# Optimization experiments

Measured on AMD Instinct MI355X. Metric: run time of the kernel, lower is better.

Reference implementation:

```python
import jax, jax.numpy as jnp
import numpy as np

H = 128
N = 100_000
VOCAB = 15_128
LAYER_TIMESTEPS = [5, 2, 5, 2]
RESIDUALS = {1: [0], 3: [1]}


def gru_cell(x, h, Wih, Whh, bih, bhh):
    # torch.nn.GRUCell semantics
    gi = x @ Wih.T + bih
    gh = h @ Whh.T + bhh
    ir, iz, inn = jnp.split(gi, 3, axis=-1)
    hr, hz, hn = jnp.split(gh, 3, axis=-1)
    r = jax.nn.sigmoid(ir + hr)
    z = jax.nn.sigmoid(iz + hz)
    n = jnp.tanh(inn + r * hn)
    return (1.0 - z) * n + z * h


def setup_inputs() -> dict:
    key = jax.random.key(0)
    ks = jax.random.split(key, 12)
    E_AST, E_MASTER, V, P = 100_000, 20_000, 30_000, 8_000
    s = 1.0 / np.sqrt(H)
    inp = {
        "node_type_ids": jax.random.randint(ks[0], (N,), 0, VOCAB),
        "edges_ast": jax.random.randint(ks[1], (E_AST, 2), 0, N),
        "edges_master": jax.random.randint(ks[2], (E_MASTER, 2), 0, N),
        "var_node_pos": jax.random.randint(ks[3], (V,), 0, N),
        "pred_node_ids": jax.random.randint(ks[4], (P,), 0, N),
        # learned params
        "embedding": jax.random.normal(ks[5], (VOCAB, H), jnp.float32) * 0.02,
        "msg_W": jax.random.normal(ks[6], (4, 4, H, H), jnp.float32) * s,  # [layer, edge_type, H, H]
        "msg_b": jnp.zeros((4, 4, H), jnp.float32),
        "Wih_a": jax.random.normal(ks[7], (2, 3 * H, H), jnp.float32) * s,      # GRU input weights, layers 0,2 (no residual)
        "Wih_b": jax.random.normal(ks[8], (2, 3 * H, 2 * H), jnp.float32) * s,  # layers 1,3 (one residual, concat -> 2H)
        "Whh": jax.random.normal(ks[9], (4, 3 * H, H), jnp.float32) * s,
        "bih": jnp.zeros((4, 3 * H), jnp.float32),
        "bhh": jnp.zeros((4, 3 * H), jnp.float32),
    }
    return inp


def reference(node_type_ids, edges_ast, edges_master, var_node_pos, pred_node_ids,
              embedding, msg_W, msg_b, Wih_a, Wih_b, Whh, bih, bhh):
    # initial node encodings via embedding lookup
    h = embedding[node_type_ids]  # [N, H]
    # 4 edge types: ast, reversed ast, var->master, master->var
    edge_lists = [edges_ast, edges_ast[:, ::-1], edges_master, edges_master[:, ::-1]]
    node_states = [h]
    num_nodes = h.shape[0]
    for layer in range(4):
        res_states = [node_states[l] for l in RESIDUALS.get(layer, [])]
        Wih = Wih_a[layer // 2] if layer in (0, 2) else Wih_b[layer // 2]
        for _ in range(LAYER_TIMESTEPS[layer]):
            incoming = jnp.zeros_like(h)
            for e, edges in enumerate(edge_lists):
                # gather source states, per-edge-type linear, scatter-add to targets
                msg = h[edges[:, 0]] @ msg_W[layer, e].T + msg_b[layer, e]
                incoming = incoming + jax.ops.segment_sum(msg, edges[:, 1], num_segments=num_nodes)
            x = jnp.concatenate([incoming] + res_states, axis=-1) if res_states else incoming
            h = gru_cell(x, h, Wih, Whh[layer], bih[layer], bhh[layer])
        node_states.append(h)
    tree_node_encoding = h
    packed_variable_encoding = tree_node_encoding[var_node_pos]
    prediction_node_encoding = tree_node_encoding[pred_node_ids]
    return tree_node_encoding, packed_variable_encoding, prediction_node_encoding
```

## Files before the change

### kernel.cpp

```cpp
#include <hip/hip_runtime.h>
#include <math.h>

#define H 128
#define NN 100000
#define E_AST 100000
#define E_MST 20000
#define E_TOT 240000
#define NV 30000
#define NP 8000
#define N4 400000
#define NH 12800000
#define VOCAB 15128

typedef unsigned short ushort_t;
typedef __attribute__((ext_vector_type(8))) unsigned short us8;
typedef _Float16 half8 __attribute__((ext_vector_type(8)));
typedef __attribute__((ext_vector_type(4))) float f32x4;

__device__ __forceinline__ unsigned short f2h(float f) {
    _Float16 h = (_Float16)f;
    return __builtin_bit_cast(unsigned short, h);
}
__device__ __forceinline__ float h2f(unsigned short u) {
    return (float)__builtin_bit_cast(_Float16, u);
}
__device__ __forceinline__ void fsplit(float x, unsigned short& hi, unsigned short& lo) {
    _Float16 a = (_Float16)x;
    _Float16 b = (_Float16)(x - (float)a);
    hi = __builtin_bit_cast(unsigned short, a);
    lo = __builtin_bit_cast(unsigned short, b);
}

#define GLD16(gsrc, ldst) __builtin_amdgcn_global_load_lds( \
    (const __attribute__((address_space(1))) unsigned int*)(gsrc), \
    (__attribute__((address_space(3))) unsigned int*)(ldst), 16, 0, 0)

__global__ void embed_kernel(const int* __restrict__ ids, const float* __restrict__ emb,
                             ushort_t* __restrict__ h16, ushort_t* __restrict__ hlo) {
    int g = blockIdx.x * 256 + threadIdx.x;
    if (g >= NN * 64) return;
    int i = g >> 6, j2 = (g & 63) << 1;
    float2 v = *(const float2*)&emb[(size_t)ids[i] * H + j2];
    unsigned short h0, l0, h1, l1;
    fsplit(v.x, h0, l0); fsplit(v.y, h1, l1);
    *(unsigned*)&h16[(size_t)i * H + j2] = (unsigned)h0 | ((unsigned)h1 << 16);
    *(unsigned*)&hlo[(size_t)i * H + j2] = (unsigned)l0 | ((unsigned)l1 << 16);
}

__device__ inline void edge_decode(int t, const int* __restrict__ ast, const int* __restrict__ mst,
                                   int& e, int& src, int& tgt) {
    if (t < E_AST)                 { e = 0; src = ast[2*t];     tgt = ast[2*t+1]; }
    else if (t < 2*E_AST)          { int i = t - E_AST;         e = 1; src = ast[2*i+1]; tgt = ast[2*i]; }
    else if (t < 2*E_AST + E_MST)  { int i = t - 2*E_AST;       e = 2; src = mst[2*i];   tgt = mst[2*i+1]; }
    else                           { int i = t - 2*E_AST-E_MST; e = 3; src = mst[2*i+1]; tgt = mst[2*i]; }
}

__global__ void count4_kernel(const int* __restrict__ ast, const int* __restrict__ mst,
                              int* __restrict__ deg4) {
    int t = blockIdx.x * 256 + threadIdx.x;
    if (t >= E_TOT) return;
    int e, src, tgt; edge_decode(t, ast, mst, e, src, tgt);
    atomicAdd(&deg4[tgt * 4 + e], 1);
}

__global__ void scan1b(const int* __restrict__ deg, int* __restrict__ excl,
                       int* __restrict__ partial, int n) {
    __shared__ int sm[256];
    int t = threadIdx.x, b = blockIdx.x;
    int base = b * 2048 + t * 8;
    int v[8]; int s = 0;
    #pragma unroll
    for (int i = 0; i < 8; ++i) { v[i] = (base + i < n) ? deg[base + i] : 0; s += v[i]; }
    sm[t] = s;
    __syncthreads();
    for (int off = 1; off < 256; off <<= 1) {
        int x = (t >= off) ? sm[t - off] : 0;
        __syncthreads();
        sm[t] += x;
        __syncthreads();
    }
    int run = sm[t] - s;
    if (t == 255) partial[b] = sm[255];
    #pragma unroll
    for (int i = 0; i < 8; ++i) {
        if (base + i < n) { excl[base + i] = run; run += v[i]; }
    }
}

__global__ void scan2(int* __restrict__ partial, int nb) {
    __shared__ int sm[256];
    int t = threadIdx.x;
    int v = (t < nb) ? partial[t] : 0;
    sm[t] = v;
    __syncthreads();
    for (int off = 1; off < 256; off <<= 1) {
        int x = (t >= off) ? sm[t - off] : 0;
        __syncthreads();
        sm[t] += x;
        __syncthreads();
    }
    if (t < nb) partial[t] = sm[t] - v;
}

__global__ void scan3b(int* __restrict__ rp, const int* __restrict__ partial, int n, int etot) {
    int i = blockIdx.x * 256 + threadIdx.x;
    if (i < n) rp[i] += partial[i >> 11];
    if (i == n) rp[n] = etot;
}

__global__ void fill4_kernel(const int* __restrict__ ast, const int* __restrict__ mst,
                             const int* __restrict__ rp4, int* __restrict__ cnt4,
                             int* __restrict__ col) {
    int t = blockIdx.x * 256 + threadIdx.x;
    if (t >= E_TOT) return;
    int e, src, tgt; edge_decode(t, ast, mst, e, src, tgt);
    int key = tgt * 4 + e;
    int slot = rp4[key] + atomicAdd(&cnt4[key], 1);
    col[slot] = src;
}

__global__ void prep_wmsg2(const float* __restrict__ W, ushort_t* __restrict__ hi,
                           ushort_t* __restrict__ lo) {
    int i = blockIdx.x * 256 + threadIdx.x;
    if (i >= 262144) return;
    fsplit(W[i], hi[i], lo[i]);
}

__global__ void prep_emb16(const float* __restrict__ emb, ushort_t* __restrict__ emb16) {
    int i = blockIdx.x * 256 + threadIdx.x;
    if (i >= VOCAB * H) return;
    emb16[i] = f2h(emb[i]);
}

__global__ void prep_B2(const float* __restrict__ Wih_a, const float* __restrict__ Wih_b,
                        const float* __restrict__ Whh,
                        ushort_t* __restrict__ B1h, ushort_t* __restrict__ B1l,
                        ushort_t* __restrict__ B2h, ushort_t* __restrict__ B2l) {
    int i = blockIdx.x * 256 + threadIdx.x;
    if (i >= 327680) return;
    int l, off, K;
    if (i < 65536)       { l = 0; off = 0;      K = 256; }
    else if (i < 163840) { l = 1; off = 65536;  K = 384; }
    else if (i < 229376) { l = 2; off = 163840; K = 256; }
    else                 { l = 3; off = 229376; K = 384; }
    int Kx = K - 128;
    const float* Wih = (l & 1) ? (Wih_b + (size_t)(l >> 1) * 384 * 256)
                               : (Wih_a + (size_t)(l >> 1) * 384 * 128);
    const float* WhhL = Whh + (size_t)l * 384 * 128;
    int rem = i - off;
    int row = rem / K, k = rem - row * K;
    int j = row >> 1, s = row & 1;
    int g1 = s * 128 + j;
    float v1 = (k < Kx) ? Wih[(size_t)g1 * Kx + k] : WhhL[(size_t)g1 * 128 + (k - Kx)];
    fsplit(v1, B1h[i], B1l[i]);
    int g2 = 256 + j;
    float v2;
    if (s == 0) v2 = (k < Kx) ? Wih[(size_t)g2 * Kx + k] : 0.f;
    else        v2 = (k < Kx) ? 0.f : WhhL[(size_t)g2 * 128 + (k - Kx)];
    fsplit(v2, B2h[i], B2l[i]);
}

__global__ __launch_bounds__(256, 4) void msg_gemm(
    const ushort_t* __restrict__ h16, const ushort_t* __restrict__ Whi,
    const ushort_t* __restrict__ Wlo, ushort_t* __restrict__ TA, ushort_t* __restrict__ TB)
{
    __shared__ ushort_t sh[16384];
    ushort_t* Ah = sh;
    ushort_t* Bs = sh + 8192;
    const int tid = threadIdx.x, w = tid >> 6, l = tid & 63;
    const int m0 = blockIdx.x * 128;
    const int n0 = blockIdx.y * 128;
    const int wm = w >> 1, wn = w & 1;
    const int lr8 = l >> 3, lslot = (l & 7) ^ lr8;
    f32x4 acc[4][4];
    #pragma unroll
    for (int a = 0; a < 4; ++a)
        #pragma unroll
        for (int b = 0; b < 4; ++b) acc[a][b] = (f32x4){0.f, 0.f, 0.f, 0.f};

    for (int kt = 0; kt < 2; ++kt) {
        const int kk = kt * 64;
        #pragma unroll
        for (int q = 0; q < 4; ++q) {
            int row8 = w * 4 + q;
            int grow = m0 + row8 * 8 + lr8; if (grow >= NN) grow = NN - 1;
            GLD16(h16 + (size_t)grow * H + kk + lslot * 8, Ah + row8 * 512);
        }
        #pragma unroll
        for (int q = 0; q < 4; ++q) {
            int row8 = w * 4 + q;
            GLD16(Whi + (size_t)(n0 + row8 * 8 + lr8) * 128 + kk + lslot * 8, Bs + row8 * 512);
        }
        __syncthreads();
        #pragma unroll
        for (int fk = 0; fk < 2; ++fk) {
            half8 av[4], bv[4];
            #pragma unroll
            for (int fm = 0; fm < 4; ++fm) {
                int row = wm * 64 + fm * 16 + (l & 15);
                int slot = (fk * 4 + (l >> 4)) ^ (row & 7);
                av[fm] = *(const half8*)&Ah[row * 64 + slot * 8];
            }
            #pragma unroll
            for (int fn = 0; fn < 4; ++fn) {
                int row = wn * 64 + fn * 16 + (l & 15);
                int slot = (fk * 4 + (l >> 4)) ^ (row & 7);
                bv[fn] = *(const half8*)&Bs[row * 64 + slot * 8];
            }
            #pragma unroll
            for (int fm = 0; fm < 4; ++fm)
                #pragma unroll
                for (int fn = 0; fn < 4; ++fn)
                    acc[fm][fn] = __builtin_amdgcn_mfma_f32_16x16x32_f16(av[fm], bv[fn], acc[fm][fn], 0, 0, 0);
        }
        __syncthreads();
        #pragma unroll
        for (int q = 0; q < 4; ++q) {
            int row8 = w * 4 + q;
            GLD16(Wlo + (size_t)(n0 + row8 * 8 + lr8) * 128 + kk + lslot * 8, Bs + row8 * 512);
        }
        __syncthreads();
        #pragma unroll
        for (int fk = 0; fk < 2; ++fk) {
            half8 av[4], bv[4];
            #pragma unroll
            for (int fm = 0; fm < 4; ++fm) {
                int row = wm * 64 + fm * 16 + (l & 15);
                int slot = (fk * 4 + (l >> 4)) ^ (row & 7);
                av[fm] = *(const half8*)&Ah[row * 64 + slot * 8];
            }
            #pragma unroll
            for (int fn = 0; fn < 4; ++fn) {
                int row = wn * 64 + fn * 16 + (l & 15);
                int slot = (fk * 4 + (l >> 4)) ^ (row & 7);
                bv[fn] = *(const half8*)&Bs[row * 64 + slot * 8];
            }
            #pragma unroll
            for (int fm = 0; fm < 4; ++fm)
                #pragma unroll
                for (int fn = 0; fn < 4; ++fn)
                    acc[fm][fn] = __builtin_amdgcn_mfma_f32_16x16x32_f16(av[fm], bv[fn], acc[fm][fn], 0, 0, 0);
        }
        __syncthreads();
    }
    #pragma unroll
    for (int fm = 0; fm < 4; ++fm)
        #pragma unroll
        for (int fn = 0; fn < 4; ++fn) {
            int colL = wn * 64 + fn * 16 + (l & 15);
            #pragma unroll
            for (int rg = 0; rg < 4; ++rg) {
                int rowL = wm * 64 + fm * 16 + (l >> 4) * 4 + rg;
                sh[rowL * 128 + colL] = f2h(acc[fm][fn][rg]);
            }
        }
    __syncthreads();
    {
        int row = tid >> 1, half = tid & 1;
        int grow = m0 + row;
        if (grow < NN) {
            ushort_t* dst = ((blockIdx.y < 2) ? TA : TB) + (size_t)grow * 256 + (blockIdx.y & 1) * 128 + half * 64;
            const ushort_t* src = &sh[row * 128 + half * 64];
            #pragma unroll
            for (int q = 0; q < 8; ++q)
                *(us8*)&dst[q * 8] = *(const us8*)&src[q * 8];
        }
    }
}

__global__ void gather_all(const ushort_t* __restrict__ TA, const ushort_t* __restrict__ TB,
                           const int* __restrict__ rp4, const int* __restrict__ col,
                           const int* __restrict__ deg4, const float* __restrict__ mb,
                           ushort_t* __restrict__ inc16) {
    int wv = threadIdx.x >> 6, l = threadIdx.x & 63;
    int t = blockIdx.x * 4 + wv;
    if (t >= NN) return;
    int c2 = l * 2;
    float a0 = 0.f, a1 = 0.f;
    #pragma unroll
    for (int e4 = 0; e4 < 4; ++e4) {
        float d = (float)deg4[t * 4 + e4];
        a0 += d * mb[e4 * H + c2];
        a1 += d * mb[e4 * H + c2 + 1];
    }
    #pragma unroll
    for (int e = 0; e < 4; ++e) {
        const ushort_t* Tb = (e < 2) ? TA : TB;
        int cb = (e & 1) * 128;
        int s0 = rp4[4 * t + e], s1 = rp4[4 * t + e + 1];
        for (int s = s0; s < s1; ++s) {
            unsigned vv = *(const unsigned*)&Tb[(size_t)col[s] * 256 + cb + c2];
            a0 += h2f((unsigned short)(vv & 0xffff));
            a1 += h2f((unsigned short)(vv >> 16));
        }
    }
    *(unsigned*)&inc16[(size_t)t * H + c2] = (unsigned)f2h(a0) | ((unsigned)f2h(a1) << 16);
}

template<int CFG>
__global__ __launch_bounds__(256, 2) void gru_fused(
    const ushort_t* __restrict__ inc16, ushort_t* __restrict__ h16, ushort_t* __restrict__ hlo,
    const ushort_t* __restrict__ s1h, const ushort_t* __restrict__ emb16, const int* __restrict__ ids,
    const ushort_t* __restrict__ B1h, const ushort_t* __restrict__ B1l,
    const ushort_t* __restrict__ B2h, const ushort_t* __restrict__ B2l,
    const float* __restrict__ bihL, const float* __restrict__ bhhL)
{
    constexpr int NPARTS = (CFG == 0) ? 2 : 3;
    constexpr int K = NPARTS * 128;
    constexpr int SLOTS = K / 8;
    constexpr int AGLD = K / 64;
    constexpr int NUNITS = NPARTS * 4;
    __shared__ ushort_t Aall[32 * K];
    __shared__ ushort_t Bs[2][256 * 64];
    const int tid = threadIdx.x, w = tid >> 6, l = tid & 63;
    const int m0 = blockIdx.x * 32;

    #pragma unroll
    for (int q = 0; q < AGLD; ++q) {
        int idx = (w * AGLD + q) * 64 + l;
        int row = idx / SLOTS;
        int s   = idx - row * SLOTS;
        int ss  = s ^ (row & 7);
        int part = ss >> 4;
        int grow = m0 + row;
        const ushort_t* sb;
        if (part == 0)                sb = inc16 + (size_t)grow * H;
        else if (part == NPARTS - 1)  sb = h16 + (size_t)grow * H;
        else                          sb = (CFG == 1) ? emb16 + (size_t)ids[grow] * H
                                                      : s1h + (size_t)grow * H;
        GLD16(sb + (ss & 15) * 8, Aall + (size_t)(w * AGLD + q) * 512);
    }

    #define STAGE_B(Bsel, p_, c_, dstbuf) { \
        _Pragma("unroll") \
        for (int q_ = 0; q_ < 8; ++q_) { \
            int row_ = (w * 8 + q_) * 8 + (l >> 3); \
            GLD16((Bsel) + (size_t)row_ * K + (p_) * 128 + (c_) * 64 + ((l & 7) ^ (l >> 3)) * 8, \
                  (dstbuf) + (w * 8 + q_) * 512); \
        } }

    STAGE_B(B1h, 0, 0, Bs[0]);
    __syncthreads();

    float rzr[2][4][4], rzz[2][4][4];
    f32x4 acc[2][4];
    #pragma unroll
    for (int a = 0; a < 2; ++a)
        #pragma unroll
        for (int b = 0; b < 4; ++b) acc[a][b] = (f32x4){0.f, 0.f, 0.f, 0.f};

    #pragma unroll
    for (int u = 0; u < 2 * NUNITS; ++u) {
        if (u + 1 < 2 * NUNITS) {
            const int un = u + 1;
            const int pass_n = (un >= NUNITS) ? 1 : 0;
            const int vn = un - pass_n * NUNITS;
            const int hl_n = vn & 1, c_n = (vn >> 1) & 1, p_n = vn >> 2;
            const ushort_t* Bsel = pass_n ? (hl_n ? B2l : B2h) : (hl_n ? B1l : B1h);
            STAGE_B(Bsel, p_n, c_n, Bs[un & 1]);
        }
        if (u == NUNITS) {
            #pragma unroll
            for (int fn = 0; fn < 4; ++fn) {
                int cc = w * 64 + fn * 16 + (l & 15);
                int j = cc >> 1, s = cc & 1;
                float bsum = s ? (bihL[128 + j] + bhhL[128 + j]) : (bihL[j] + bhhL[j]);
                #pragma unroll
                for (int fm = 0; fm < 2; ++fm)
                    #pragma unroll
                    for (int rg = 0; rg < 4; ++rg) {
                        float g = 1.f / (1.f + __expf(-(acc[fm][fn][rg] + bsum)));
                        float other = __shfl_xor(g, 1);
                        rzr[fm][fn][rg] = s ? other : g;
                        rzz[fm][fn][rg] = s ? g : other;
                        acc[fm][fn][rg] = 0.f;
                    }
            }
        }
        {
            const int pass = (u >= NUNITS) ? 1 : 0;
            const int v = u - pass * NUNITS;
            const int c = (v >> 1) & 1, p = v >> 2;
            #pragma unroll
            for (int fk = 0; fk < 2; ++fk) {
                half8 av[2], bv[4];
                #pragma unroll
                for (int fm = 0; fm < 2; ++fm) {
                    int Ra = fm * 16 + (l & 15);
                    int slot = (p * 16 + c * 8 + fk * 4 + (l >> 4)) ^ (Ra & 7);
                    av[fm] = *(const half8*)&Aall[(size_t)Ra * K + slot * 8];
                }
                #pragma unroll
                for (int fn = 0; fn < 4; ++fn) {
                    int Rb = w * 64 + fn * 16 + (l & 15);
                    int slot = (fk * 4 + (l >> 4)) ^ (Rb & 7);
                    bv[fn] = *(const half8*)&Bs[u & 1][(size_t)Rb * 64 + slot * 8];
                }
                #pragma unroll
                for (int fm = 0; fm < 2; ++fm)
                    #pragma unroll
                    for (int fn = 0; fn < 4; ++fn)
                        acc[fm][fn] = __builtin_amdgcn_mfma_f32_16x16x32_f16(av[fm], bv[fn], acc[fm][fn], 0, 0, 0);
            }
        }
        __syncthreads();
    }
    #undef STAGE_B

    ushort_t* ohi = Bs[0];
    ushort_t* olo = Bs[0] + 4096;
    #pragma unroll
    for (int fn = 0; fn < 4; ++fn) {
        int cc = w * 64 + fn * 16 + (l & 15);
        int j = cc >> 1, s = cc & 1;
        float bsum = s ? bhhL[256 + j] : bihL[256 + j];
        #pragma unroll
        for (int fm = 0; fm < 2; ++fm)
            #pragma unroll
            for (int rg = 0; rg < 4; ++rg) {
                float self = acc[fm][fn][rg] + bsum;
                float other = __shfl_xor(self, 1);
                if (s == 0) {
                    int rl = fm * 16 + (l >> 4) * 4 + rg;
                    int row = m0 + rl;
                    float n = tanhf(self + rzr[fm][fn][rg] * other);
                    float hold = h2f(h16[(size_t)row * H + j]) + h2f(hlo[(size_t)row * H + j]);
                    float z = rzz[fm][fn][rg];
                    float o = (1.f - z) * n + z * hold;
                    unsigned short hi, lo;
                    fsplit(o, hi, lo);
                    ohi[rl * 128 + j] = hi;
                    olo[rl * 128 + j] = lo;
                }
            }
    }
    __syncthreads();
    {
        int row = tid >> 3, seg = tid & 7;
        size_t go = (size_t)(m0 + row) * H + seg * 16;
        *(us8*)&h16[go]     = *(const us8*)&ohi[row * 128 + seg * 16];
        *(us8*)&h16[go + 8] = *(const us8*)&ohi[row * 128 + seg * 16 + 8];
        *(us8*)&hlo[go]     = *(const us8*)&olo[row * 128 + seg * 16];
        *(us8*)&hlo[go + 8] = *(const us8*)&olo[row * 128 + seg * 16 + 8];
    }
}

__global__ void recon_kernel(const ushort_t* __restrict__ h16, const ushort_t* __restrict__ hlo,
                             float* __restrict__ out) {
    int g = blockIdx.x * 256 + threadIdx.x;
    if (g >= NN * 64) return;
    unsigned hi2 = *(const unsigned*)&h16[(size_t)g * 2];
    unsigned lo2 = *(const unsigned*)&hlo[(size_t)g * 2];
    float2 o;
    o.x = h2f((unsigned short)(hi2 & 0xffff)) + h2f((unsigned short)(lo2 & 0xffff));
    o.y = h2f((unsigned short)(hi2 >> 16)) + h2f((unsigned short)(lo2 >> 16));
    *(float2*)&out[(size_t)g * 2] = o;
}

__global__ void out_gather(const float* __restrict__ h, const int* __restrict__ idx,
                           float* __restrict__ out, int n) {
    int g = blockIdx.x * 256 + threadIdx.x;
    if (g >= n * 64) return;
    int v = g >> 6, j2 = (g & 63) << 1;
    *(float2*)&out[(size_t)v * H + j2] = *(const float2*)&h[(size_t)idx[v] * H + j2];
}

extern "C" void kernel_launch(void* const* d_in, const int* in_sizes, int n_in,
                              void* d_out, int out_size, void* d_ws, size_t ws_size,
                              hipStream_t stream) {
    const int*   ids    = (const int*)d_in[0];
    const int*   ast    = (const int*)d_in[1];
    const int*   mst    = (const int*)d_in[2];
    const int*   varpos = (const int*)d_in[3];
    const int*   predid = (const int*)d_in[4];
    const float* emb    = (const float*)d_in[5];
    const float* msg_W  = (const float*)d_in[6];
    const float* msg_b  = (const float*)d_in[7];
    const float* Wih_a  = (const float*)d_in[8];
    const float* Wih_b  = (const float*)d_in[9];
    const float* Whh    = (const float*)d_in[10];
    const float* bih    = (const float*)d_in[11];
    const float* bhh    = (const float*)d_in[12];

    float* out = (float*)d_out;
    ushort_t* TB = (ushort_t*)out;

    int* ibase = (int*)(out + NH);
    int* deg4  = ibase;
    int* rp4   = ibase + 400000;
    int* cnt4  = ibase + 800001;
    int* col   = ibase + 1200001;
    int* part  = ibase + 1440001;
    ushort_t* WT    = (ushort_t*)(ibase + 1500000);
    ushort_t* wmh   = WT;
    ushort_t* wml   = WT + 262144;
    ushort_t* B1h   = WT + 524288;
    ushort_t* B1l   = WT + 851968;
    ushort_t* B2h   = WT + 1179648;
    ushort_t* B2l   = WT + 1507328;
    ushort_t* emb16 = WT + 1835008;

    if (ws_size < (size_t)153600000) return;
    char* wsb = (char*)d_ws;
    ushort_t* h16   = (ushort_t*)wsb;
    ushort_t* hlo   = (ushort_t*)(wsb + 25600000);
    ushort_t* s1h   = (ushort_t*)(wsb + 51200000);
    ushort_t* inc16 = (ushort_t*)(wsb + 76800000);
    ushort_t* TA    = (ushort_t*)(wsb + 102400000);

    embed_kernel<<<25000, 256, 0, stream>>>(ids, emb, h16, hlo);

    hipMemsetAsync(deg4, 0, N4 * sizeof(int), stream);
    hipMemsetAsync(cnt4, 0, N4 * sizeof(int), stream);
    count4_kernel<<<(E_TOT + 255) / 256, 256, 0, stream>>>(ast, mst, deg4);
    scan1b<<<196, 256, 0, stream>>>(deg4, rp4, part, N4);
    scan2<<<1, 256, 0, stream>>>(part, 196);
    scan3b<<<1563, 256, 0, stream>>>(rp4, part, N4, E_TOT);
    fill4_kernel<<<(E_TOT + 255) / 256, 256, 0, stream>>>(ast, mst, rp4, cnt4, col);
    prep_wmsg2<<<1024, 256, 0, stream>>>(msg_W, wmh, wml);
    prep_B2<<<1280, 256, 0, stream>>>(Wih_a, Wih_b, Whh, B1h, B1l, B2h, B2l);
    prep_emb16<<<7564, 256, 0, stream>>>(emb, emb16);

    const int LT[4] = {5, 2, 5, 2};
    const int Boff[4] = {0, 65536, 163840, 229376};
    for (int layer = 0; layer < 4; ++layer) {
        const float* bihL = bih + layer * 384;
        const float* bhhL = bhh + layer * 384;
        const float* mbL  = msg_b + (size_t)layer * 512;
        const ushort_t* wmhL = wmh + (size_t)layer * 65536;
        const ushort_t* wmlL = wml + (size_t)layer * 65536;
        const ushort_t* B1hL = B1h + Boff[layer];
        const ushort_t* B1lL = B1l + Boff[layer];
        const ushort_t* B2hL = B2h + Boff[layer];
        const ushort_t* B2lL = B2l + Boff[layer];

        for (int ts = 0; ts < LT[layer]; ++ts) {
            msg_gemm<<<dim3(782, 4), 256, 0, stream>>>(h16, wmhL, wmlL, TA, TB);
            gather_all<<<25000, 256, 0, stream>>>(TA, TB, rp4, col, deg4, mbL, inc16);
            if (layer == 0 || layer == 2)
                gru_fused<0><<<3125, 256, 0, stream>>>(inc16, h16, hlo, s1h, emb16, ids,
                    B1hL, B1lL, B2hL, B2lL, bihL, bhhL);
            else if (layer == 1)
                gru_fused<1><<<3125, 256, 0, stream>>>(inc16, h16, hlo, s1h, emb16, ids,
                    B1hL, B1lL, B2hL, B2lL, bihL, bhhL);
            else
                gru_fused<2><<<3125, 256, 0, stream>>>(inc16, h16, hlo, s1h, emb16, ids,
                    B1hL, B1lL, B2hL, B2lL, bihL, bhhL);
        }
        if (layer == 0)
            hipMemcpyAsync(s1h, h16, (size_t)NH * 2, hipMemcpyDeviceToDevice, stream);
    }

    recon_kernel<<<25000, 256, 0, stream>>>(h16, hlo, out);
    out_gather<<<(NV * 64 + 255) / 256, 256, 0, stream>>>(out, varpos, out + NH, NV);
    out_gather<<<(NP * 64 + 255) / 256, 256, 0, stream>>>(out, predid, out + NH + (size_t)NV * H, NP);
}
```

Baseline: 4.416 ms.

## Pre-swizzle GRU weights into MFMA fragment layout and load B directly from global

Rewrites the GRU weight prep so the weights are stored in per-wave MFMA B-fragment order, with r/z/in/hn columns interleaved in groups of four. The GRU kernel then reads B fragments straight from global/L2 instead of staging them through double-buffered LDS with barriers. It also merges the two passes (r/z gates, then n gates) into one pass over 512 columns, using shuffles to bring the gate values together. This drops the LDS B staging and the per-unit syncthreads and frees LDS, which allows 3 blocks per CU instead of 2. The cost is more accumulator registers (acc[2][8]) and B-fragment loads that now come from global memory on every block.

```diff
diff --git a/kernel.cpp b/kernel.cpp
--- a/kernel.cpp
+++ b/kernel.cpp
@@ -132,32 +132,39 @@
     emb16[i] = f2h(emb[i]);
 }
 
-__global__ void prep_B2(const float* __restrict__ Wih_a, const float* __restrict__ Wih_b,
-                        const float* __restrict__ Whh,
-                        ushort_t* __restrict__ B1h, ushort_t* __restrict__ B1l,
-                        ushort_t* __restrict__ B2h, ushort_t* __restrict__ B2l) {
-    int i = blockIdx.x * 256 + threadIdx.x;
-    if (i >= 327680) return;
-    int l, off, K;
-    if (i < 65536)       { l = 0; off = 0;      K = 256; }
-    else if (i < 163840) { l = 1; off = 65536;  K = 384; }
-    else if (i < 229376) { l = 2; off = 163840; K = 256; }
-    else                 { l = 3; off = 229376; K = 384; }
-    int Kx = K - 128;
-    const float* Wih = (l & 1) ? (Wih_b + (size_t)(l >> 1) * 384 * 256)
-                               : (Wih_a + (size_t)(l >> 1) * 384 * 128);
-    const float* WhhL = Whh + (size_t)l * 384 * 128;
-    int rem = i - off;
-    int row = rem / K, k = rem - row * K;
-    int j = row >> 1, s = row & 1;
-    int g1 = s * 128 + j;
-    float v1 = (k < Kx) ? Wih[(size_t)g1 * Kx + k] : WhhL[(size_t)g1 * 128 + (k - Kx)];
-    fsplit(v1, B1h[i], B1l[i]);
-    int g2 = 256 + j;
-    float v2;
-    if (s == 0) v2 = (k < Kx) ? Wih[(size_t)g2 * Kx + k] : 0.f;
-    else        v2 = (k < Kx) ? 0.f : WhhL[(size_t)g2 * 128 + (k - Kx)];
-    fsplit(v2, B2h[i], B2l[i]);
+__global__ void prep_Bfrag(const float* __restrict__ Wih_a, const float* __restrict__ Wih_b,
+                           const float* __restrict__ Whh, ushort_t* __restrict__ Bfrag) {
+    int idx = blockIdx.x * 256 + threadIdx.x;
+    if (idx >= 1310720) return;
+    int layer, off, NPARTS;
+    if (idx < 262144)       { layer = 0; off = 0;      NPARTS = 2; }
+    else if (idx < 655360)  { layer = 1; off = 262144; NPARTS = 3; }
+    else if (idx < 917504)  { layer = 2; off = 655360; NPARTS = 2; }
+    else                    { layer = 3; off = 917504; NPARTS = 3; }
+    int rem = idx - off;
+    int e  = rem & 7;
+    int l  = (rem >> 3) & 63;
+    int fn = (rem >> 9) & 7;
+    int fk = (rem >> 12) & 1;
+    int w  = (rem >> 13) & 3;
+    int unit = rem >> 15;
+    int hl = unit & 1, c = (unit >> 1) & 1, p = unit >> 2;
+
+    int Kx = (NPARTS - 1) * 128;
+    const float* Wih = (layer & 1) ? (Wih_b + (size_t)(layer >> 1) * 384 * 256)
+                                   : (Wih_a + (size_t)(layer >> 1) * 384 * 128);
+    const float* WhhL = Whh + (size_t)layer * 384 * 128;
+
+    int col = w * 128 + fn * 16 + (l & 15);
+    int s = col & 3, j = col >> 2;
+    int k = p * 128 + c * 64 + fk * 32 + (l >> 4) * 8 + e;
+    int grow = (s == 0) ? j : (s == 1) ? 128 + j : 256 + j;
+    float val;
+    if (k < Kx) val = (s == 3) ? 0.f : Wih[(size_t)grow * Kx + k];
+    else        val = (s == 2) ? 0.f : WhhL[(size_t)grow * 128 + (k - Kx)];
+    unsigned short hi, lo;
+    fsplit(val, hi, lo);
+    Bfrag[idx] = hl ? lo : hi;
 }
 
 __global__ __launch_bounds__(256, 4) void msg_gemm(
@@ -298,20 +305,18 @@
 }
 
 template<int CFG>
-__global__ __launch_bounds__(256, 2) void gru_fused(
+__global__ __launch_bounds__(256, 3) void gru_fused(
     const ushort_t* __restrict__ inc16, ushort_t* __restrict__ h16, ushort_t* __restrict__ hlo,
     const ushort_t* __restrict__ s1h, const ushort_t* __restrict__ emb16, const int* __restrict__ ids,
-    const ushort_t* __restrict__ B1h, const ushort_t* __restrict__ B1l,
-    const ushort_t* __restrict__ B2h, const ushort_t* __restrict__ B2l,
+    const ushort_t* __restrict__ Bfrag,
     const float* __restrict__ bihL, const float* __restrict__ bhhL)
 {
     constexpr int NPARTS = (CFG == 0) ? 2 : 3;
     constexpr int K = NPARTS * 128;
     constexpr int SLOTS = K / 8;
     constexpr int AGLD = K / 64;
-    constexpr int NUNITS = NPARTS * 4;
     __shared__ ushort_t Aall[32 * K];
-    __shared__ ushort_t Bs[2][256 * 64];
+    __shared__ ushort_t osh[8192];
     const int tid = threadIdx.x, w = tid >> 6, l = tid & 63;
     const int m0 = blockIdx.x * 32;
 
@@ -330,102 +335,67 @@
                                                       : s1h + (size_t)grow * H;
         GLD16(sb + (ss & 15) * 8, Aall + (size_t)(w * AGLD + q) * 512);
     }
-
-    #define STAGE_B(Bsel, p_, c_, dstbuf) { \
-        _Pragma("unroll") \
-        for (int q_ = 0; q_ < 8; ++q_) { \
-            int row_ = (w * 8 + q_) * 8 + (l >> 3); \
-            GLD16((Bsel) + (size_t)row_ * K + (p_) * 128 + (c_) * 64 + ((l & 7) ^ (l >> 3)) * 8, \
-                  (dstbuf) + (w * 8 + q_) * 512); \
-        } }
-
-    STAGE_B(B1h, 0, 0, Bs[0]);
     __syncthreads();
 
-    float rzr[2][4][4], rzz[2][4][4];
-    f32x4 acc[2][4];
+    f32x4 acc[2][8];
     #pragma unroll
     for (int a = 0; a < 2; ++a)
         #pragma unroll
-        for (int b = 0; b < 4; ++b) acc[a][b] = (f32x4){0.f, 0.f, 0.f, 0.f};
-
-    #pragma unroll
-    for (int u = 0; u < 2 * NUNITS; ++u) {
-        if (u + 1 < 2 * NUNITS) {
-            const int un = u + 1;
-            const int pass_n = (un >= NUNITS) ? 1 : 0;
-            const int vn = un - pass_n * NUNITS;
-            const int hl_n = vn & 1, c_n = (vn >> 1) & 1, p_n = vn >> 2;
-            const ushort_t* Bsel = pass_n ? (hl_n ? B2l : B2h) : (hl_n ? B1l : B1h);
-            STAGE_B(Bsel, p_n, c_n, Bs[un & 1]);
-        }
-        if (u == NUNITS) {
-            #pragma unroll
-            for (int fn = 0; fn < 4; ++fn) {
-                int cc = w * 64 + fn * 16 + (l & 15);
-                int j = cc >> 1, s = cc & 1;
-                float bsum = s ? (bihL[128 + j] + bhhL[128 + j]) : (bihL[j] + bhhL[j]);
+        for (int b = 0; b < 8; ++b) acc[a][b] = (f32x4){0.f, 0.f, 0.f, 0.f};
+
+    #pragma unroll
+    for (int p = 0; p < NPARTS; ++p)
+        #pragma unroll
+        for (int c = 0; c < 2; ++c)
+            #pragma unroll
+            for (int hl = 0; hl < 2; ++hl) {
+                const int unit = (p * 2 + c) * 2 + hl;
+                const ushort_t* bu = Bfrag + (size_t)(unit * 4 + w) * 8192;
                 #pragma unroll
-                for (int fm = 0; fm < 2; ++fm)
+                for (int fk = 0; fk < 2; ++fk) {
+                    half8 av[2], bv[8];
                     #pragma unroll
-                    for (int rg = 0; rg < 4; ++rg) {
-                        float g = 1.f / (1.f + __expf(-(acc[fm][fn][rg] + bsum)));
-                        float other = __shfl_xor(g, 1);
-                        rzr[fm][fn][rg] = s ? other : g;
-                        rzz[fm][fn][rg] = s ? g : other;
-                        acc[fm][fn][rg] = 0.f;
+                    for (int fm = 0; fm < 2; ++fm) {
+                        int Ra = fm * 16 + (l & 15);
+                        int sk = p * 16 + c * 8 + fk * 4 + (l >> 4);
+                        int slot = sk ^ (Ra & 7);
+                        av[fm] = *(const half8*)&Aall[(size_t)Ra * K + slot * 8];
                     }
-            }
-        }
-        {
-            const int pass = (u >= NUNITS) ? 1 : 0;
-            const int v = u - pass * NUNITS;
-            const int c = (v >> 1) & 1, p = v >> 2;
-            #pragma unroll
-            for (int fk = 0; fk < 2; ++fk) {
-                half8 av[2], bv[4];
-                #pragma unroll
-                for (int fm = 0; fm < 2; ++fm) {
-                    int Ra = fm * 16 + (l & 15);
-                    int slot = (p * 16 + c * 8 + fk * 4 + (l >> 4)) ^ (Ra & 7);
-                    av[fm] = *(const half8*)&Aall[(size_t)Ra * K + slot * 8];
+                    #pragma unroll
+                    for (int fn = 0; fn < 8; ++fn)
+                        bv[fn] = *(const half8*)&bu[((size_t)fk * 8 + fn) * 512 + l * 8];
+                    #pragma unroll
+                    for (int fm = 0; fm < 2; ++fm)
+                        #pragma unroll
+                        for (int fn = 0; fn < 8; ++fn)
+                            acc[fm][fn] = __builtin_amdgcn_mfma_f32_16x16x32_f16(av[fm], bv[fn], acc[fm][fn], 0, 0, 0);
                 }
-                #pragma unroll
-                for (int fn = 0; fn < 4; ++fn) {
-                    int Rb = w * 64 + fn * 16 + (l & 15);
-                    int slot = (fk * 4 + (l >> 4)) ^ (Rb & 7);
-                    bv[fn] = *(const half8*)&Bs[u & 1][(size_t)Rb * 64 + slot * 8];
-                }
-                #pragma unroll
-                for (int fm = 0; fm < 2; ++fm)
-                    #pragma unroll
-                    for (int fn = 0; fn < 4; ++fn)
-                        acc[fm][fn] = __builtin_amdgcn_mfma_f32_16x16x32_f16(av[fm], bv[fn], acc[fm][fn], 0, 0, 0);
-            }
-        }
-        __syncthreads();
-    }
-    #undef STAGE_B
-
-    ushort_t* ohi = Bs[0];
-    ushort_t* olo = Bs[0] + 4096;
-    #pragma unroll
-    for (int fn = 0; fn < 4; ++fn) {
-        int cc = w * 64 + fn * 16 + (l & 15);
-        int j = cc >> 1, s = cc & 1;
-        float bsum = s ? bhhL[256 + j] : bihL[256 + j];
+            }
+
+    ushort_t* ohi = osh;
+    ushort_t* olo = osh + 4096;
+    #pragma unroll
+    for (int fn = 0; fn < 8; ++fn) {
+        int cc = w * 128 + fn * 16 + (l & 15);
+        int j = cc >> 2, s = cc & 3;
+        float bsum = (s == 0) ? bihL[j] + bhhL[j]
+                   : (s == 1) ? bihL[128 + j] + bhhL[128 + j]
+                   : (s == 2) ? bihL[256 + j] : bhhL[256 + j];
         #pragma unroll
         for (int fm = 0; fm < 2; ++fm)
             #pragma unroll
             for (int rg = 0; rg < 4; ++rg) {
-                float self = acc[fm][fn][rg] + bsum;
-                float other = __shfl_xor(self, 1);
+                float pre = acc[fm][fn][rg] + bsum;
+                float g = (s < 2) ? 1.f / (1.f + __expf(-pre)) : pre;
+                float o1 = __shfl_xor(g, 1);
+                float o2 = __shfl_xor(g, 2);
+                float o3 = __shfl_xor(o1, 2);
                 if (s == 0) {
                     int rl = fm * 16 + (l >> 4) * 4 + rg;
                     int row = m0 + rl;
-                    float n = tanhf(self + rzr[fm][fn][rg] * other);
+                    float r = g, z = o1, inn = o2, hn = o3;
+                    float n = tanhf(inn + r * hn);
                     float hold = h2f(h16[(size_t)row * H + j]) + h2f(hlo[(size_t)row * H + j]);
-                    float z = rzz[fm][fn][rg];
                     float o = (1.f - z) * n + z * hold;
                     unsigned short hi, lo;
                     fsplit(o, hi, lo);
@@ -494,11 +464,8 @@
     ushort_t* WT    = (ushort_t*)(ibase + 1500000);
     ushort_t* wmh   = WT;
     ushort_t* wml   = WT + 262144;
-    ushort_t* B1h   = WT + 524288;
-    ushort_t* B1l   = WT + 851968;
-    ushort_t* B2h   = WT + 1179648;
-    ushort_t* B2l   = WT + 1507328;
-    ushort_t* emb16 = WT + 1835008;
+    ushort_t* emb16 = WT + 524288;
+    ushort_t* Bfrag = WT + 2460672;
 
     if (ws_size < (size_t)153600000) return;
     char* wsb = (char*)d_ws;
@@ -518,34 +485,31 @@
     scan3b<<<1563, 256, 0, stream>>>(rp4, part, N4, E_TOT);
     fill4_kernel<<<(E_TOT + 255) / 256, 256, 0, stream>>>(ast, mst, rp4, cnt4, col);
     prep_wmsg2<<<1024, 256, 0, stream>>>(msg_W, wmh, wml);
-    prep_B2<<<1280, 256, 0, stream>>>(Wih_a, Wih_b, Whh, B1h, B1l, B2h, B2l);
     prep_emb16<<<7564, 256, 0, stream>>>(emb, emb16);
+    prep_Bfrag<<<5120, 256, 0, stream>>>(Wih_a, Wih_b, Whh, Bfrag);
 
     const int LT[4] = {5, 2, 5, 2};
-    const int Boff[4] = {0, 65536, 163840, 229376};
+    const size_t Foff[4] = {0, 262144, 655360, 917504};
     for (int layer = 0; layer < 4; ++layer) {
         const float* bihL = bih + layer * 384;
         const float* bhhL = bhh + layer * 384;
         const float* mbL  = msg_b + (size_t)layer * 512;
         const ushort_t* wmhL = wmh + (size_t)layer * 65536;
         const ushort_t* wmlL = wml + (size_t)layer * 65536;
-        const ushort_t* B1hL = B1h + Boff[layer];
-        const ushort_t* B1lL = B1l + Boff[layer];
-        const ushort_t* B2hL = B2h + Boff[layer];
-        const ushort_t* B2lL = B2l + Boff[layer];
+        const ushort_t* BfL  = Bfrag + Foff[layer];
 
         for (int ts = 0; ts < LT[layer]; ++ts) {
             msg_gemm<<<dim3(782, 4), 256, 0, stream>>>(h16, wmhL, wmlL, TA, TB);
             gather_all<<<25000, 256, 0, stream>>>(TA, TB, rp4, col, deg4, mbL, inc16);
             if (layer == 0 || layer == 2)
                 gru_fused<0><<<3125, 256, 0, stream>>>(inc16, h16, hlo, s1h, emb16, ids,
-                    B1hL, B1lL, B2hL, B2lL, bihL, bhhL);
+                    BfL, bihL, bhhL);
             else if (layer == 1)
                 gru_fused<1><<<3125, 256, 0, stream>>>(inc16, h16, hlo, s1h, emb16, ids,
-                    B1hL, B1lL, B2hL, B2lL, bihL, bhhL);
+                    BfL, bihL, bhhL);
             else
                 gru_fused<2><<<3125, 256, 0, stream>>>(inc16, h16, hlo, s1h, emb16, ids,
-                    B1hL, B1lL, B2hL, B2lL, bihL, bhhL);
+                    BfL, bihL, bhhL);
         }
         if (layer == 0)
             hipMemcpyAsync(s1h, h16, (size_t)NH * 2, hipMemcpyDeviceToDevice, stream);
```

Result: faster. 4.188 ms (-5.2%).
